# Performance work log

Measured on AMD Instinct MI355X. Metric: run time of the kernel, lower is better.

## Reference

```python
import jax, jax.numpy as jnp
import numpy as np

TEMP = 1.0

def setup_inputs() -> dict:
    key = jax.random.key(0)
    k1, k2 = jax.random.split(key)
    B, T, C, Vp1 = 16, 2048, 256, 1025
    z = jax.random.normal(k1, (B, T, C), dtype=jnp.float32)
    mask = jnp.ones((B, T, 1), dtype=jnp.float32)
    codebook_weight = jax.random.normal(k2, (Vp1, C), dtype=jnp.float32)
    return {"z": z, "mask": mask, "codebook_weight": codebook_weight}

def reference(z, mask, codebook_weight):
    # e = codebook.embedding.weight.clone().detach()[1:, :]
    e = jax.lax.stop_gradient(codebook_weight[1:, :])  # [V, C]
    b, t, c = z.shape
    V = e.shape[0]
    z_flat = z.reshape(-1, c)                          # [N, C], N = b*t
    # sim(): cosine-sim matmul + log_softmax + argmax one-hot quantize
    cos_sim = jnp.matmul(z_flat, e.T)                  # [N, V]
    log_probs = jax.nn.log_softmax(cos_sim / TEMP, axis=1)
    indices = jnp.argmax(log_probs, axis=1)            # [N]
    # one_hot @ e is exactly a row gather -- avoid materializing one_hot
    z_q = e[indices]                                   # [N, C]
    z_q3 = z_q.reshape(b, t, c)
    # loss(): masked commitment + smoothness
    valid_count = mask.sum() * c
    commitment_loss = (jnp.square(z - jax.lax.stop_gradient(z_q3)) * mask).sum() / valid_count
    smoothness_loss = (jnp.square(z[:, :-1, :] - z[:, 1:, :]) * mask[:, 1:, :]).sum() / valid_count
    # codebook_usage(): (one_hot * mask).sum(0) / mask.sum(), normalized
    mflat = mask.reshape(-1)                           # [N]
    prob = jax.ops.segment_sum(mflat, indices, num_segments=V) / mflat.sum()
    e_mean = prob / prob.sum()
    return (smoothness_loss, commitment_loss, log_probs.reshape(b, t, V), z_q3, e_mean)
```

## Files before the change

kernel.cpp:

```cpp
#include <hip/hip_runtime.h>
#include <hip/hip_bf16.h>

#define TPB 256
#define TPB2 512
#define BM 32
#define NROW 32768
#define NBLK (NROW / BM)
#define VV 1024
#define KD 256
#define TT 2048

#define LP_OFF 2L
#define ZQ_OFF (2L + 33554432L)
#define EM_OFF (33554434L + 8388608L)

#define WS_HIST 0
#define WS_CSUM 1024
#define WS_SSUM 2048
#define WS_MSUM 3072
#define WS_E8 4096
#define WS_NEED (4096 * 4 + 32 * 1024 * 8 * 2)

typedef __attribute__((ext_vector_type(8))) short bf16x8;
typedef __attribute__((ext_vector_type(4))) float f32x4;

__device__ __forceinline__ void gl_lds16(const float* g, float* l) {
  __builtin_amdgcn_global_load_lds(
      (const __attribute__((address_space(1))) void*)g,
      (__attribute__((address_space(3))) void*)l, 16, 0, 0);
}

__device__ __forceinline__ unsigned short f2bf(float x) {
  unsigned u = __float_as_uint(x);
  unsigned r = ((u >> 16) & 1u) + 0x7FFFu;
  return (unsigned short)((u + r) >> 16);
}

__global__ __launch_bounds__(256) void tok_prep(const float* __restrict__ cw,
                                                unsigned short* __restrict__ e8) {
  int t = blockIdx.x * 256 + threadIdx.x;
  int o = t >> 10, n = t & 1023;
  const float* src = cw + (size_t)(1 + n) * KD + (o << 3);
  float4 a = *(const float4*)src;
  float4 b = *(const float4*)(src + 4);
  int4 pk;
  pk.x = f2bf(a.x) | ((unsigned)f2bf(a.y) << 16);
  pk.y = f2bf(a.z) | ((unsigned)f2bf(a.w) << 16);
  pk.z = f2bf(b.x) | ((unsigned)f2bf(b.y) << 16);
  pk.w = f2bf(b.z) | ((unsigned)f2bf(b.w) << 16);
  *(int4*)(e8 + (((size_t)(o << 10) + n) << 3)) = pk;
}

__global__ __launch_bounds__(TPB2, 2) void tok_mfma(
    const float* __restrict__ z, const float* __restrict__ mask,
    const float* __restrict__ cw, const unsigned short* __restrict__ e8,
    float* __restrict__ out, float* __restrict__ ws) {
  __shared__ __align__(16) float z_s[BM][KD];
  __shared__ __align__(16) unsigned short z8[32][32][8];
  __shared__ unsigned wkey[32][8][4];
  __shared__ float wmax[32][8];
  __shared__ float wsum[32][8];
  __shared__ float exv[32][4];
  __shared__ int exi[32][4];
  __shared__ int argi[32];
  __shared__ float cred[8], sred[8];

  const int tid = threadIdx.x;
  const int lane = tid & 63;
  const int w = tid >> 6;
  const int g = lane >> 4;
  const int lm = lane & 15;
  const int c0 = w << 7;
  const int n0 = blockIdx.x * BM;

#pragma unroll
  for (int i = 0; i < 4; ++i) {
    int row = (i << 3) + w;
    gl_lds16(&z[(size_t)(n0 + row) * KD + (lane << 2)], &z_s[row][lane << 2]);
  }
  __syncthreads();
#pragma unroll
  for (int i = 0; i < 2; ++i) {
    int e = (i << 9) + tid;
    int o = e >> 5, r = e & 31;
    float4 a = *(const float4*)&z_s[r][o << 3];
    float4 b = *(const float4*)&z_s[r][(o << 3) + 4];
    int4 pk;
    pk.x = f2bf(a.x) | ((unsigned)f2bf(a.y) << 16);
    pk.y = f2bf(a.z) | ((unsigned)f2bf(a.w) << 16);
    pk.z = f2bf(b.x) | ((unsigned)f2bf(b.y) << 16);
    pk.w = f2bf(b.z) | ((unsigned)f2bf(b.w) << 16);
    *(int4*)&z8[o][r][0] = pk;
  }
  __syncthreads();

  const bf16x8* za = (const bf16x8*)&z8[0][0][0];
  const bf16x8* bb = (const bf16x8*)e8 + (g << 10) + c0 + lm;
  f32x4 accA[8], accB[8];
  const f32x4 zz = {0.f, 0.f, 0.f, 0.f};
#pragma unroll
  for (int nt = 0; nt < 8; ++nt) { accA[nt] = zz; accB[nt] = zz; }
#pragma unroll 2
  for (int step = 0; step < 8; ++step) {
    bf16x8 a0 = za[(step << 7) + (g << 5) + lm];
    bf16x8 a1 = za[(step << 7) + (g << 5) + 16 + lm];
#pragma unroll
    for (int nt = 0; nt < 8; ++nt) {
      bf16x8 bv = bb[(step << 12) + (nt << 4)];
      accA[nt] = __builtin_amdgcn_mfma_f32_16x16x32_bf16(a0, bv, accA[nt], 0, 0, 0);
      accB[nt] = __builtin_amdgcn_mfma_f32_16x16x32_bf16(a1, bv, accB[nt], 0, 0, 0);
    }
  }

  auto phase1 = [&](f32x4(&ac)[8], int mt) {
#pragma unroll
    for (int j = 0; j < 4; ++j) {
      int r = (mt << 4) + (g << 2) + j;
      float mv = -3.4e38f;
      unsigned cur[8];
#pragma unroll
      for (int nt = 0; nt < 8; ++nt) {
        float v = ac[nt][j];
        mv = fmaxf(mv, v);
        unsigned b = __float_as_uint(v);
        b ^= (unsigned)((int)b >> 31) | 0x80000000u;
        cur[nt] = (b & 0xFFFFFC00u) |
                  (1023u - (unsigned)(c0 + (nt << 4) + lm));
      }
#pragma unroll
      for (int d = 1; d <= 8; d <<= 1) mv = fmaxf(mv, __shfl_xor(mv, d));
      if (lm == 0) wmax[r][w] = mv;
#pragma unroll
      for (int t2 = 0; t2 < 4; ++t2) {
        unsigned mk = cur[0];
#pragma unroll
        for (int nt = 1; nt < 8; ++nt) mk = mk > cur[nt] ? mk : cur[nt];
#pragma unroll
        for (int d = 1; d <= 8; d <<= 1) {
          unsigned o2 = __shfl_xor(mk, d);
          mk = mk > o2 ? mk : o2;
        }
        if (lm == 0) wkey[r][w][t2] = mk;
#pragma unroll
        for (int nt = 0; nt < 8; ++nt)
          if (cur[nt] == mk) cur[nt] = 0;
      }
    }
  };
  phase1(accA, 0);
  phase1(accB, 1);
  __syncthreads();

  auto phase2 = [&](f32x4(&ac)[8], int mt) {
#pragma unroll
    for (int j = 0; j < 4; ++j) {
      int r = (mt << 4) + (g << 2) + j;
      float M = wmax[r][0];
#pragma unroll
      for (int w2 = 1; w2 < 8; ++w2) M = fmaxf(M, wmax[r][w2]);
      float s = 0.f;
#pragma unroll
      for (int nt = 0; nt < 8; ++nt) s += __expf(ac[nt][j] - M);
#pragma unroll
      for (int d = 1; d <= 8; d <<= 1) s += __shfl_xor(s, d);
      if (lm == 0) wsum[r][w] = s;
    }
  };
  phase2(accA, 0);
  phase2(accB, 1);
  __syncthreads();

  auto phase3 = [&](f32x4(&ac)[8], int mt) {
#pragma unroll
    for (int j = 0; j < 4; ++j) {
      int r = (mt << 4) + (g << 2) + j;
      float M = wmax[r][0];
#pragma unroll
      for (int w2 = 1; w2 < 8; ++w2) M = fmaxf(M, wmax[r][w2]);
      float S = 0.f;
#pragma unroll
      for (int w2 = 0; w2 < 8; ++w2) S += wsum[r][w2];
      float lse = M + __logf(S);
      size_t base = LP_OFF + (size_t)(n0 + r) * VV;
#pragma unroll
      for (int nt = 0; nt < 8; ++nt)
        out[base + c0 + (nt << 4) + lm] = ac[nt][j] - lse;
    }
  };
  phase3(accA, 0);
  phase3(accB, 1);

  const int r4 = w << 2;
#pragma unroll
  for (int rr = 0; rr < 4; ++rr) {
    int row = r4 + rr;
    unsigned key = (lane < 32) ? wkey[row][lane >> 2][lane & 3] : 0u;
#pragma unroll
    for (int t2 = 0; t2 < 4; ++t2) {
      unsigned mk = key;
#pragma unroll
      for (int d = 1; d <= 32; d <<= 1) {
        unsigned o2 = __shfl_xor(mk, d);
        mk = mk > o2 ? mk : o2;
      }
      exi[row][t2] = (int)(1023u - (mk & 0x3FFu));
      if (key == mk) key = 0;
    }
  }
#pragma unroll
  for (int p = 0; p < 2; ++p) {
    int row = r4 + (p << 1) + (lane >> 5);
    int cd = (lane >> 3) & 3;
    int cand = exi[row][cd];
    int seg = lane & 7;
    const float* er = cw + (size_t)(1 + cand) * KD + (seg << 5);
    const float* zr = &z_s[row][seg << 5];
    float s = 0.f;
#pragma unroll
    for (int i2 = 0; i2 < 8; ++i2) {
      float4 a4 = *(const float4*)(zr + (i2 << 2));
      float4 b4 = *(const float4*)(er + (i2 << 2));
      s += a4.x * b4.x + a4.y * b4.y + a4.z * b4.z + a4.w * b4.w;
    }
    s += __shfl_xor(s, 1);
    s += __shfl_xor(s, 2);
    s += __shfl_xor(s, 4);
    if (seg == 0) exv[row][cd] = s;
  }
  __syncthreads();
  if (tid < 32) {
    int row = tid;
    float bv = exv[row][0];
    int bi = exi[row][0];
#pragma unroll
    for (int c = 1; c < 4; ++c) {
      float v = exv[row][c];
      int ci = exi[row][c];
      if (v > bv || (v == bv && ci < bi)) { bv = v; bi = ci; }
    }
    argi[row] = bi;
    atomicAdd(&ws[WS_HIST + bi], mask[n0 + row]);
  }
  __syncthreads();

  float csum = 0.f, ssum = 0.f;
  const bool has_prev = (n0 % TT) != 0;
#pragma unroll
  for (int i = 0; i < 4; ++i) {
    int q = i * TPB2 + tid;
    int r = q >> 6;
    int c4 = (q & 63) << 2;
    int idx = argi[r];
    const float4 ev = *(const float4*)&cw[(size_t)(1 + idx) * KD + c4];
    const float4 zv = *(const float4*)&z_s[r][c4];
    *(float4*)&out[ZQ_OFF + (size_t)(n0 + r) * KD + c4] = ev;
    float mk = mask[n0 + r];
    float dx = zv.x - ev.x, dy = zv.y - ev.y, dz2 = zv.z - ev.z,
          dw = zv.w - ev.w;
    csum += mk * (dx * dx + dy * dy + dz2 * dz2 + dw * dw);
    if (r > 0) {
      const float4 pv = *(const float4*)&z_s[r - 1][c4];
      float ax = zv.x - pv.x, ay = zv.y - pv.y, az = zv.z - pv.z,
            aw = zv.w - pv.w;
      ssum += mk * (ax * ax + ay * ay + az * az + aw * aw);
    } else if (has_prev) {
      const float4 pv = *(const float4*)&z[(size_t)(n0 - 1) * KD + c4];
      float ax = zv.x - pv.x, ay = zv.y - pv.y, az = zv.z - pv.z,
            aw = zv.w - pv.w;
      ssum += mk * (ax * ax + ay * ay + az * az + aw * aw);
    }
  }
#pragma unroll
  for (int d = 1; d <= 32; d <<= 1) {
    csum += __shfl_xor(csum, d);
    ssum += __shfl_xor(ssum, d);
  }
  if (lane == 0) { cred[w] = csum; sred[w] = ssum; }
  __syncthreads();
  if (tid == 0) {
    float cs = 0.f, ss2 = 0.f;
#pragma unroll
    for (int i = 0; i < 8; ++i) { cs += cred[i]; ss2 += sred[i]; }
    ws[WS_CSUM + blockIdx.x] = cs;
    ws[WS_SSUM + blockIdx.x] = ss2;
    float ms = 0.f;
    for (int r2 = 0; r2 < BM; ++r2) ms += mask[n0 + r2];
    ws[WS_MSUM + blockIdx.x] = ms;
  }
}

__global__ __launch_bounds__(TPB, 2) void tok_fb(
    const float* __restrict__ z, const float* __restrict__ mask,
    const float* __restrict__ cw, float* __restrict__ out,
    float* __restrict__ ws) {
  __shared__ __align__(16) float z_s[BM][KD];
  __shared__ int argi_s[BM];
  __shared__ float cred[4], sred[4];
  const int tid = threadIdx.x;
  const int lane = tid & 63;
  const int wave = tid >> 6;
  const int n0 = blockIdx.x * BM;
  const float* e = cw + KD;
#pragma unroll
  for (int i = 0; i < 8; ++i) {
    int seg = wave * 8 + i;
    gl_lds16(&z[(size_t)(n0 + seg) * KD + lane * 4], &z_s[seg][0]);
  }
  __syncthreads();
  float acc[8][16];
#pragma unroll
  for (int r = 0; r < 8; ++r)
#pragma unroll
    for (int m = 0; m < 16; ++m) acc[r][m] = 0.f;
#pragma unroll 1
  for (int i = 0; i < 64; ++i) {
    float4 ef[16];
#pragma unroll
    for (int m = 0; m < 16; ++m)
      ef[m] = *(const float4*)&e[(size_t)((m << 6) + lane) * KD + (i << 2)];
    float4 zf[8];
#pragma unroll
    for (int rr = 0; rr < 8; ++rr)
      zf[rr] = *(const float4*)&z_s[(wave << 3) + rr][i << 2];
#pragma unroll
    for (int m = 0; m < 16; ++m)
#pragma unroll
      for (int rr = 0; rr < 8; ++rr)
        acc[rr][m] += zf[rr].x * ef[m].x + zf[rr].y * ef[m].y +
                      zf[rr].z * ef[m].z + zf[rr].w * ef[m].w;
  }
  const int rowbase = wave << 3;
#pragma unroll
  for (int rr = 0; rr < 8; ++rr) {
    float mv = acc[rr][0];
    int mc = lane;
#pragma unroll
    for (int m = 1; m < 16; ++m) {
      float v = acc[rr][m];
      int c = (m << 6) + lane;
      bool tk = v > mv;
      mc = tk ? c : mc;
      mv = tk ? v : mv;
    }
#pragma unroll
    for (int d = 32; d >= 1; d >>= 1) {
      float ov = __shfl_xor(mv, d);
      int oc = __shfl_xor(mc, d);
      bool tk = (ov > mv) || (ov == mv && oc < mc);
      mv = tk ? ov : mv;
      mc = tk ? oc : mc;
    }
    float sum = 0.f;
#pragma unroll
    for (int m = 0; m < 16; ++m) sum += __expf(acc[rr][m] - mv);
#pragma unroll
    for (int d = 32; d >= 1; d >>= 1) sum += __shfl_xor(sum, d);
    float lse = mv + __logf(sum);
    size_t base = LP_OFF + (size_t)(n0 + rowbase + rr) * VV;
#pragma unroll
    for (int m = 0; m < 16; ++m) out[base + (m << 6) + lane] = acc[rr][m] - lse;
    if (lane == 0) {
      argi_s[rowbase + rr] = mc;
      atomicAdd(&ws[WS_HIST + mc], mask[n0 + rowbase + rr]);
    }
  }
  __syncthreads();
  float csum = 0.f, ssum = 0.f;
  const bool has_prev = (n0 % TT) != 0;
#pragma unroll
  for (int i = 0; i < 8; ++i) {
    int q = i * TPB + tid;
    int r = q >> 6;
    int c4 = (q & 63) << 2;
    int idx = argi_s[r];
    const float4 ev = *(const float4*)&e[(size_t)idx * KD + c4];
    const float4 zv = *(const float4*)&z_s[r][c4];
    *(float4*)&out[ZQ_OFF + (size_t)(n0 + r) * KD + c4] = ev;
    float mk = mask[n0 + r];
    float dx = zv.x - ev.x, dy = zv.y - ev.y, dz2 = zv.z - ev.z, dw = zv.w - ev.w;
    csum += mk * (dx * dx + dy * dy + dz2 * dz2 + dw * dw);
    if (r > 0) {
      const float4 pv = *(const float4*)&z_s[r - 1][c4];
      float ax = zv.x - pv.x, ay = zv.y - pv.y, az = zv.z - pv.z, aw = zv.w - pv.w;
      ssum += mk * (ax * ax + ay * ay + az * az + aw * aw);
    } else if (has_prev) {
      const float4 pv = *(const float4*)&z[(size_t)(n0 - 1) * KD + c4];
      float ax = zv.x - pv.x, ay = zv.y - pv.y, az = zv.z - pv.z, aw = zv.w - pv.w;
      ssum += mk * (ax * ax + ay * ay + az * az + aw * aw);
    }
  }
#pragma unroll
  for (int d = 32; d >= 1; d >>= 1) {
    csum += __shfl_xor(csum, d);
    ssum += __shfl_xor(ssum, d);
  }
  if (lane == 0) { cred[wave] = csum; sred[wave] = ssum; }
  __syncthreads();
  if (tid == 0) {
    ws[WS_CSUM + blockIdx.x] = cred[0] + cred[1] + cred[2] + cred[3];
    ws[WS_SSUM + blockIdx.x] = sred[0] + sred[1] + sred[2] + sred[3];
    float ms = 0.f;
    for (int r2 = 0; r2 < BM; ++r2) ms += mask[n0 + r2];
    ws[WS_MSUM + blockIdx.x] = ms;
  }
}

__global__ __launch_bounds__(1024) void tok_final(const float* __restrict__ ws,
                                                  float* __restrict__ out) {
  const int t = threadIdx.x;
  const int lane = t & 63, w = t >> 6;
  __shared__ float red[16];
  auto blockReduce = [&](float v) -> float {
#pragma unroll
    for (int d = 32; d >= 1; d >>= 1) v += __shfl_xor(v, d);
    __syncthreads();
    if (lane == 0) red[w] = v;
    __syncthreads();
    float s = 0.f;
#pragma unroll
    for (int i = 0; i < 16; ++i) s += red[i];
    return s;
  };
  float Mtot = blockReduce(ws[WS_MSUM + t]);
  float Ctot = blockReduce(ws[WS_CSUM + t]);
  float Stot = blockReduce(ws[WS_SSUM + t]);
  float prob = ws[WS_HIST + t] / Mtot;
  float psum = blockReduce(prob);
  out[EM_OFF + t] = prob / psum;
  if (t == 0) {
    float vc = Mtot * (float)KD;
    out[0] = Stot / vc;
    out[1] = Ctot / vc;
  }
}

extern "C" void kernel_launch(void* const* d_in, const int* in_sizes, int n_in,
                              void* d_out, int out_size, void* d_ws,
                              size_t ws_size, hipStream_t stream) {
  const float* z = (const float*)d_in[0];
  const float* mask = (const float*)d_in[1];
  const float* cw = (const float*)d_in[2];
  float* out = (float*)d_out;
  float* ws = (float*)d_ws;
  hipMemsetAsync(ws, 0, 1024 * sizeof(float), stream);
  if (ws_size >= (size_t)WS_NEED) {
    unsigned short* e8 = (unsigned short*)(ws + WS_E8);
    tok_prep<<<128, 256, 0, stream>>>(cw, e8);
    tok_mfma<<<NBLK, TPB2, 0, stream>>>(z, mask, cw, e8, out, ws);
  } else {
    tok_fb<<<NBLK, TPB, 0, stream>>>(z, mask, cw, out, ws);
  }
  tok_final<<<1, 1024, 0, stream>>>(ws, out);
}
```

Before: 103.5 us.

## Widen MFMA kernel to 16 waves with swizzled codebook layout and register prefetch

The main kernel now uses 1024 threads (16 waves), each covering 64 vocabulary columns instead of 128. The bf16 codebook is repacked into a per-wave contiguous layout, and B-operand fragments are prefetched two k-steps ahead in registers. The z bf16 tile in LDS is XOR-swizzled to avoid bank conflicts. The row max now comes from the top-1 argmax keys instead of a separate float max pass, each wave keeps a top-2 candidate list instead of top-4, and mask values are cached in LDS. The aim is more latency hiding and fewer redundant reductions, at the cost of extra barriers and a smaller per-wave candidate set.

```diff
diff --git a/kernel.cpp b/kernel.cpp
--- a/kernel.cpp
+++ b/kernel.cpp
@@ -1,8 +1,7 @@
 #include <hip/hip_runtime.h>
 #include <hip/hip_bf16.h>
 
-#define TPB 256
-#define TPB2 512
+#define TPB 1024
 #define BM 32
 #define NROW 32768
 #define NBLK (NROW / BM)
@@ -36,8 +35,17 @@
   return (unsigned short)((u + r) >> 16);
 }
 
-__global__ __launch_bounds__(256) void tok_prep(const float* __restrict__ cw,
-                                                unsigned short* __restrict__ e8) {
+__device__ __forceinline__ unsigned foldf(float v) {
+  unsigned b = __float_as_uint(v);
+  return b ^ ((unsigned)((int)b >> 31) | 0x80000000u);
+}
+__device__ __forceinline__ float unfoldf(unsigned k) {
+  unsigned s = (unsigned)((int)k >> 31);
+  return __uint_as_float(k ^ (0x80000000u | (~s & 0x7FFFFFFFu)));
+}
+
+__global__ __launch_bounds__(256) void tok_prep(
+    const float* __restrict__ cw, unsigned short* __restrict__ e8) {
   int t = blockIdx.x * 256 + threadIdx.x;
   int o = t >> 10, n = t & 1023;
   const float* src = cw + (size_t)(1 + n) * KD + (o << 3);
@@ -48,41 +56,41 @@
   pk.y = f2bf(a.z) | ((unsigned)f2bf(a.w) << 16);
   pk.z = f2bf(b.x) | ((unsigned)f2bf(b.y) << 16);
   pk.w = f2bf(b.z) | ((unsigned)f2bf(b.w) << 16);
-  *(int4*)(e8 + (((size_t)(o << 10) + n) << 3)) = pk;
-}
-
-__global__ __launch_bounds__(TPB2, 2) void tok_mfma(
+  int U = ((n >> 6) << 11) + ((o >> 2) << 8) + (((n >> 4) & 3) << 6) +
+          ((o & 3) << 4) + (n & 15);
+  *(int4*)(e8 + ((size_t)U << 3)) = pk;
+}
+
+__global__ __launch_bounds__(TPB, 4) void tok_mfma(
     const float* __restrict__ z, const float* __restrict__ mask,
     const float* __restrict__ cw, const unsigned short* __restrict__ e8,
     float* __restrict__ out, float* __restrict__ ws) {
-  __shared__ __align__(16) float z_s[BM][KD];
-  __shared__ __align__(16) unsigned short z8[32][32][8];
-  __shared__ unsigned wkey[32][8][4];
-  __shared__ float wmax[32][8];
-  __shared__ float wsum[32][8];
-  __shared__ float exv[32][4];
-  __shared__ int exi[32][4];
+  __shared__ __align__(16) float z_s[BM][260];
+  __shared__ __align__(16) unsigned short z8u[8192];
+  __shared__ unsigned wkey[16][2][33];
+  __shared__ float wsum_s[16][33];
+  __shared__ float Mrow_s[32], lse_s[32];
+  __shared__ float exv_s[32][4];
+  __shared__ int exi_s[32][4];
   __shared__ int argi[32];
-  __shared__ float cred[8], sred[8];
+  __shared__ float mask_s[32];
+  __shared__ float cred[16], sred[16];
 
   const int tid = threadIdx.x;
   const int lane = tid & 63;
   const int w = tid >> 6;
   const int g = lane >> 4;
   const int lm = lane & 15;
-  const int c0 = w << 7;
+  const int c0 = w << 6;
   const int n0 = blockIdx.x * BM;
 
-#pragma unroll
-  for (int i = 0; i < 4; ++i) {
-    int row = (i << 3) + w;
-    gl_lds16(&z[(size_t)(n0 + row) * KD + (lane << 2)], &z_s[row][lane << 2]);
-  }
-  __syncthreads();
-#pragma unroll
-  for (int i = 0; i < 2; ++i) {
-    int e = (i << 9) + tid;
-    int o = e >> 5, r = e & 31;
+  gl_lds16(&z[(size_t)(n0 + w) * KD + (lane << 2)], &z_s[w][0]);
+  gl_lds16(&z[(size_t)(n0 + 16 + w) * KD + (lane << 2)], &z_s[16 + w][0]);
+  if (tid < 32) mask_s[tid] = mask[n0 + tid];
+  __syncthreads();
+
+  {
+    int r = tid >> 5, o = tid & 31;
     float4 a = *(const float4*)&z_s[r][o << 3];
     float4 b = *(const float4*)&z_s[r][(o << 3) + 4];
     int4 pk;
@@ -90,60 +98,75 @@
     pk.y = f2bf(a.z) | ((unsigned)f2bf(a.w) << 16);
     pk.z = f2bf(b.x) | ((unsigned)f2bf(b.y) << 16);
     pk.w = f2bf(b.z) | ((unsigned)f2bf(b.w) << 16);
-    *(int4*)&z8[o][r][0] = pk;
-  }
-  __syncthreads();
-
-  const bf16x8* za = (const bf16x8*)&z8[0][0][0];
-  const bf16x8* bb = (const bf16x8*)e8 + (g << 10) + c0 + lm;
-  f32x4 accA[8], accB[8];
+    *(int4*)&z8u[(unsigned)(((o << 5) + (r ^ ((o & 7) << 2))) << 3)] = pk;
+  }
+  __syncthreads();
+
+  const bf16x8* za = (const bf16x8*)z8u;
+  const bf16x8* bb = (const bf16x8*)e8 + (w << 11) + (g << 4) + lm;
+  f32x4 accA[4], accB[4];
   const f32x4 zz = {0.f, 0.f, 0.f, 0.f};
 #pragma unroll
-  for (int nt = 0; nt < 8; ++nt) { accA[nt] = zz; accB[nt] = zz; }
-#pragma unroll 2
+  for (int nt = 0; nt < 4; ++nt) { accA[nt] = zz; accB[nt] = zz; }
+  bf16x8 bA[4], bB[4], bC[4];
+#pragma unroll
+  for (int nt = 0; nt < 4; ++nt) bA[nt] = bb[nt << 6];
+#pragma unroll
+  for (int nt = 0; nt < 4; ++nt) bB[nt] = bb[256 + (nt << 6)];
+#pragma unroll
   for (int step = 0; step < 8; ++step) {
-    bf16x8 a0 = za[(step << 7) + (g << 5) + lm];
-    bf16x8 a1 = za[(step << 7) + (g << 5) + 16 + lm];
-#pragma unroll
-    for (int nt = 0; nt < 8; ++nt) {
-      bf16x8 bv = bb[(step << 12) + (nt << 4)];
-      accA[nt] = __builtin_amdgcn_mfma_f32_16x16x32_bf16(a0, bv, accA[nt], 0, 0, 0);
-      accB[nt] = __builtin_amdgcn_mfma_f32_16x16x32_bf16(a1, bv, accB[nt], 0, 0, 0);
-    }
-  }
-
-  auto phase1 = [&](f32x4(&ac)[8], int mt) {
+    if (step < 6) {
+#pragma unroll
+      for (int nt = 0; nt < 4; ++nt) bC[nt] = bb[((step + 2) << 8) + (nt << 6)];
+    }
+    const int oct = (step << 2) + g;
+    const int sw = (oct & 7) << 2;
+    bf16x8 a0 = za[(oct << 5) + (lm ^ sw)];
+    bf16x8 a1 = za[(oct << 5) + ((16 + lm) ^ sw)];
+#pragma unroll
+    for (int nt = 0; nt < 4; ++nt) {
+      accA[nt] = __builtin_amdgcn_mfma_f32_16x16x32_bf16(a0, bA[nt], accA[nt], 0, 0, 0);
+      accB[nt] = __builtin_amdgcn_mfma_f32_16x16x32_bf16(a1, bA[nt], accB[nt], 0, 0, 0);
+    }
+#pragma unroll
+    for (int nt = 0; nt < 4; ++nt) { bA[nt] = bB[nt]; bB[nt] = bC[nt]; }
+  }
+
+  unsigned colpack[4];
+#pragma unroll
+  for (int nt = 0; nt < 4; ++nt)
+    colpack[nt] = 1023u - (unsigned)(c0 + (nt << 4) + lm);
+
+  auto phase1 = [&](f32x4(&ac)[4], int mt) {
 #pragma unroll
     for (int j = 0; j < 4; ++j) {
       int r = (mt << 4) + (g << 2) + j;
-      float mv = -3.4e38f;
-      unsigned cur[8];
-#pragma unroll
-      for (int nt = 0; nt < 8; ++nt) {
-        float v = ac[nt][j];
-        mv = fmaxf(mv, v);
-        unsigned b = __float_as_uint(v);
-        b ^= (unsigned)((int)b >> 31) | 0x80000000u;
-        cur[nt] = (b & 0xFFFFFC00u) |
-                  (1023u - (unsigned)(c0 + (nt << 4) + lm));
+      unsigned cur[4];
+#pragma unroll
+      for (int nt = 0; nt < 4; ++nt)
+        cur[nt] = (foldf(ac[nt][j]) & 0xFFFFFC00u) | colpack[nt];
+      unsigned k1 = cur[0];
+#pragma unroll
+      for (int nt = 1; nt < 4; ++nt) k1 = k1 > cur[nt] ? k1 : cur[nt];
+#pragma unroll
+      for (int d = 1; d <= 8; d <<= 1) {
+        unsigned o2 = __shfl_xor(k1, d);
+        k1 = k1 > o2 ? k1 : o2;
       }
 #pragma unroll
-      for (int d = 1; d <= 8; d <<= 1) mv = fmaxf(mv, __shfl_xor(mv, d));
-      if (lm == 0) wmax[r][w] = mv;
-#pragma unroll
-      for (int t2 = 0; t2 < 4; ++t2) {
-        unsigned mk = cur[0];
-#pragma unroll
-        for (int nt = 1; nt < 8; ++nt) mk = mk > cur[nt] ? mk : cur[nt];
-#pragma unroll
-        for (int d = 1; d <= 8; d <<= 1) {
-          unsigned o2 = __shfl_xor(mk, d);
-          mk = mk > o2 ? mk : o2;
-        }
-        if (lm == 0) wkey[r][w][t2] = mk;
-#pragma unroll
-        for (int nt = 0; nt < 8; ++nt)
-          if (cur[nt] == mk) cur[nt] = 0;
+      for (int nt = 0; nt < 4; ++nt)
+        if (cur[nt] == k1) cur[nt] = 0u;
+      unsigned k2 = cur[0];
+#pragma unroll
+      for (int nt = 1; nt < 4; ++nt) k2 = k2 > cur[nt] ? k2 : cur[nt];
+#pragma unroll
+      for (int d = 1; d <= 8; d <<= 1) {
+        unsigned o2 = __shfl_xor(k2, d);
+        k2 = k2 > o2 ? k2 : o2;
+      }
+      if (lm == 0) {
+        wkey[w][0][r] = k1;
+        wkey[w][1][r] = k2;
       }
     }
   };
@@ -151,50 +174,62 @@
   phase1(accB, 1);
   __syncthreads();
 
-  auto phase2 = [&](f32x4(&ac)[8], int mt) {
+  if (tid < 32) {
+    int r = tid;
+    unsigned mk = wkey[0][0][r];
+#pragma unroll
+    for (int w2 = 1; w2 < 16; ++w2) {
+      unsigned k = wkey[w2][0][r];
+      mk = mk > k ? mk : k;
+    }
+    Mrow_s[r] = unfoldf(mk & 0xFFFFFC00u);
+  }
+  __syncthreads();
+
+  auto phase2 = [&](f32x4(&ac)[4], int mt) {
 #pragma unroll
     for (int j = 0; j < 4; ++j) {
       int r = (mt << 4) + (g << 2) + j;
-      float M = wmax[r][0];
-#pragma unroll
-      for (int w2 = 1; w2 < 8; ++w2) M = fmaxf(M, wmax[r][w2]);
+      float M = Mrow_s[r];
       float s = 0.f;
 #pragma unroll
-      for (int nt = 0; nt < 8; ++nt) s += __expf(ac[nt][j] - M);
+      for (int nt = 0; nt < 4; ++nt) s += __expf(ac[nt][j] - M);
 #pragma unroll
       for (int d = 1; d <= 8; d <<= 1) s += __shfl_xor(s, d);
-      if (lm == 0) wsum[r][w] = s;
+      if (lm == 0) wsum_s[w][r] = s;
     }
   };
   phase2(accA, 0);
   phase2(accB, 1);
   __syncthreads();
 
-  auto phase3 = [&](f32x4(&ac)[8], int mt) {
+  if (tid < 32) {
+    int r = tid;
+    float S = 0.f;
+#pragma unroll
+    for (int w2 = 0; w2 < 16; ++w2) S += wsum_s[w2][r];
+    lse_s[r] = Mrow_s[r] + __logf(S);
+  }
+  __syncthreads();
+
+  auto phase3 = [&](f32x4(&ac)[4], int mt) {
 #pragma unroll
     for (int j = 0; j < 4; ++j) {
       int r = (mt << 4) + (g << 2) + j;
-      float M = wmax[r][0];
-#pragma unroll
-      for (int w2 = 1; w2 < 8; ++w2) M = fmaxf(M, wmax[r][w2]);
-      float S = 0.f;
-#pragma unroll
-      for (int w2 = 0; w2 < 8; ++w2) S += wsum[r][w2];
-      float lse = M + __logf(S);
+      float lse = lse_s[r];
       size_t base = LP_OFF + (size_t)(n0 + r) * VV;
 #pragma unroll
-      for (int nt = 0; nt < 8; ++nt)
+      for (int nt = 0; nt < 4; ++nt)
         out[base + c0 + (nt << 4) + lm] = ac[nt][j] - lse;
     }
   };
   phase3(accA, 0);
   phase3(accB, 1);
 
-  const int r4 = w << 2;
-#pragma unroll
-  for (int rr = 0; rr < 4; ++rr) {
-    int row = r4 + rr;
-    unsigned key = (lane < 32) ? wkey[row][lane >> 2][lane & 3] : 0u;
+#pragma unroll
+  for (int rr = 0; rr < 2; ++rr) {
+    int row = (w << 1) + rr;
+    unsigned key = (lane < 32) ? wkey[lane >> 1][lane & 1][row] : 0u;
 #pragma unroll
     for (int t2 = 0; t2 < 4; ++t2) {
       unsigned mk = key;
@@ -203,16 +238,18 @@
         unsigned o2 = __shfl_xor(mk, d);
         mk = mk > o2 ? mk : o2;
       }
-      exi[row][t2] = (int)(1023u - (mk & 0x3FFu));
-      if (key == mk) key = 0;
-    }
-  }
-#pragma unroll
-  for (int p = 0; p < 2; ++p) {
-    int row = r4 + (p << 1) + (lane >> 5);
-    int cd = (lane >> 3) & 3;
-    int cand = exi[row][cd];
+      if (lane == 0) exi_s[row][t2] = (int)(1023u - (mk & 0x3FFu));
+      if (key == mk) key = 0u;
+    }
+  }
+  __syncthreads();
+
+  {
+    int p = lane >> 3;
     int seg = lane & 7;
+    int row = (w << 1) + (p >> 2);
+    int cd = p & 3;
+    int cand = exi_s[row][cd];
     const float* er = cw + (size_t)(1 + cand) * KD + (seg << 5);
     const float* zr = &z_s[row][seg << 5];
     float s = 0.f;
@@ -225,36 +262,37 @@
     s += __shfl_xor(s, 1);
     s += __shfl_xor(s, 2);
     s += __shfl_xor(s, 4);
-    if (seg == 0) exv[row][cd] = s;
-  }
-  __syncthreads();
+    if (seg == 0) exv_s[row][cd] = s;
+  }
+  __syncthreads();
+
   if (tid < 32) {
     int row = tid;
-    float bv = exv[row][0];
-    int bi = exi[row][0];
+    float bv = exv_s[row][0];
+    int bi = exi_s[row][0];
 #pragma unroll
     for (int c = 1; c < 4; ++c) {
-      float v = exv[row][c];
-      int ci = exi[row][c];
+      float v = exv_s[row][c];
+      int ci = exi_s[row][c];
       if (v > bv || (v == bv && ci < bi)) { bv = v; bi = ci; }
     }
     argi[row] = bi;
-    atomicAdd(&ws[WS_HIST + bi], mask[n0 + row]);
+    atomicAdd(&ws[WS_HIST + bi], mask_s[row]);
   }
   __syncthreads();
 
   float csum = 0.f, ssum = 0.f;
   const bool has_prev = (n0 % TT) != 0;
 #pragma unroll
-  for (int i = 0; i < 4; ++i) {
-    int q = i * TPB2 + tid;
+  for (int i = 0; i < 2; ++i) {
+    int q = i * TPB + tid;
     int r = q >> 6;
     int c4 = (q & 63) << 2;
     int idx = argi[r];
     const float4 ev = *(const float4*)&cw[(size_t)(1 + idx) * KD + c4];
     const float4 zv = *(const float4*)&z_s[r][c4];
     *(float4*)&out[ZQ_OFF + (size_t)(n0 + r) * KD + c4] = ev;
-    float mk = mask[n0 + r];
+    float mk = mask_s[r];
     float dx = zv.x - ev.x, dy = zv.y - ev.y, dz2 = zv.z - ev.z,
           dw = zv.w - ev.w;
     csum += mk * (dx * dx + dy * dy + dz2 * dz2 + dw * dw);
@@ -280,16 +318,16 @@
   if (tid == 0) {
     float cs = 0.f, ss2 = 0.f;
 #pragma unroll
-    for (int i = 0; i < 8; ++i) { cs += cred[i]; ss2 += sred[i]; }
+    for (int i = 0; i < 16; ++i) { cs += cred[i]; ss2 += sred[i]; }
     ws[WS_CSUM + blockIdx.x] = cs;
     ws[WS_SSUM + blockIdx.x] = ss2;
     float ms = 0.f;
-    for (int r2 = 0; r2 < BM; ++r2) ms += mask[n0 + r2];
+    for (int r2 = 0; r2 < BM; ++r2) ms += mask_s[r2];
     ws[WS_MSUM + blockIdx.x] = ms;
   }
 }
 
-__global__ __launch_bounds__(TPB, 2) void tok_fb(
+__global__ __launch_bounds__(256, 2) void tok_fb(
     const float* __restrict__ z, const float* __restrict__ mask,
     const float* __restrict__ cw, float* __restrict__ out,
     float* __restrict__ ws) {
@@ -369,7 +407,7 @@
   const bool has_prev = (n0 % TT) != 0;
 #pragma unroll
   for (int i = 0; i < 8; ++i) {
-    int q = i * TPB + tid;
+    int q = i * 256 + tid;
     int r = q >> 6;
     int c4 = (q & 63) << 2;
     int idx = argi_s[r];
@@ -446,9 +484,9 @@
   if (ws_size >= (size_t)WS_NEED) {
     unsigned short* e8 = (unsigned short*)(ws + WS_E8);
     tok_prep<<<128, 256, 0, stream>>>(cw, e8);
-    tok_mfma<<<NBLK, TPB2, 0, stream>>>(z, mask, cw, e8, out, ws);
+    tok_mfma<<<NBLK, TPB, 0, stream>>>(z, mask, cw, e8, out, ws);
   } else {
-    tok_fb<<<NBLK, TPB, 0, stream>>>(z, mask, cw, out, ws);
+    tok_fb<<<NBLK, 256, 0, stream>>>(z, mask, cw, out, ws);
   }
   tok_final<<<1, 1024, 0, stream>>>(ws, out);
 }
```

Result: slower. 123.2 us (+19.0%).
